# Kernel tuning notes

Measured on AMD Instinct MI355X. Metric: run time of the kernel, lower is better.

Reference implementation:

```python
import jax, jax.numpy as jnp
import numpy as np

N_POINTS = 32768
K = 16
N_EDGES = N_POINTS * K
IN_CH, OUT_CH = 3, 1
HID, LIFT, PROJ = 64, 256, 256
N_LAYERS = 4
POS_DIM = 2


def _lin_init(key, fan_in, fan_out):
    return jax.random.normal(key, (fan_in, fan_out), jnp.float32) / np.sqrt(fan_in)


def setup_inputs() -> dict:
    key = jax.random.key(0)
    ks = jax.random.split(key, 16)
    x = jax.random.normal(ks[0], (2, N_POINTS, IN_CH), jnp.float32)
    pos = jax.random.uniform(ks[1], (N_POINTS, POS_DIM), jnp.float32)
    edge_index = jax.random.randint(ks[2], (2, N_EDGES), 0, N_POINTS, jnp.int64)
    eff_in = IN_CH + POS_DIM
    kin = HID + 2 * POS_DIM  # concat(pos_src, pos_dst, x_src)
    return {
        "x": x,
        "pos": pos,
        "edge_index": edge_index,
        "lift_w1": _lin_init(ks[3], eff_in, LIFT),
        "lift_b1": jnp.zeros((LIFT,), jnp.float32),
        "lift_w2": _lin_init(ks[4], LIFT, HID),
        "lift_b2": jnp.zeros((HID,), jnp.float32),
        "kW1": jax.random.normal(ks[5], (N_LAYERS, kin, HID), jnp.float32) / np.sqrt(kin),
        "kb1": jnp.zeros((N_LAYERS, HID), jnp.float32),
        "kW2": jax.random.normal(ks[6], (N_LAYERS, HID, HID), jnp.float32) / np.sqrt(HID),
        "kb2": jnp.zeros((N_LAYERS, HID), jnp.float32),
        "proj_w1": _lin_init(ks[7], HID, PROJ),
        "proj_b1": jnp.zeros((PROJ,), jnp.float32),
        "proj_w2": _lin_init(ks[8], PROJ, OUT_CH),
        "proj_b2": jnp.zeros((OUT_CH,), jnp.float32),
    }


def _gelu(v):
    return jax.nn.gelu(v, approximate=False)  # torch nn.GELU default (exact)


def reference(x, pos, edge_index, lift_w1, lift_b1, lift_w2, lift_b2,
              kW1, kb1, kW2, kb2, proj_w1, proj_b1, proj_w2, proj_b2):
    B, n, _ = x.shape
    posb = jnp.broadcast_to(pos[None], (B, n, pos.shape[-1]))
    # lift: Linear -> GELU -> Linear on concat([x, pos])
    h = jnp.concatenate([x, posb], axis=-1)
    h = _gelu(h @ lift_w1 + lift_b1) @ lift_w2 + lift_b2  # [B, n, HID]

    src, dst = edge_index[0], edge_index[1]
    pos_e = jnp.concatenate([pos[src], pos[dst]], axis=-1)  # [E, 2*POS_DIM]
    cnt = jax.ops.segment_sum(jnp.ones((src.shape[0],), h.dtype), dst, num_segments=n)
    cnt = jnp.maximum(cnt, 1.0)[None, :, None]

    for l in range(kW1.shape[0]):
        xj = h[:, src]  # gather neighbor features [B, E, HID]
        e = jnp.concatenate([jnp.broadcast_to(pos_e[None], (B,) + pos_e.shape), xj], axis=-1)
        m = _gelu(e @ kW1[l] + kb1[l]) @ kW2[l] + kb2[l]  # edge messages [B, E, HID]
        agg = jax.vmap(lambda mb: jax.ops.segment_sum(mb, dst, num_segments=n))(m)
        h = h + agg / cnt  # mean aggregation + residual skip

    out = _gelu(h @ proj_w1 + proj_b1) @ proj_w2 + proj_b2  # [B, n, OUT_CH]
    return out.transpose(0, 2, 1)  # [B, OUT_CH, n]
```

## Files before the change

kernel.cpp:

```cpp
#include <hip/hip_runtime.h>
#include <cstdint>
#include <cstddef>

#define N_POINTS 32768
#define KDEG 16
#define N_EDGES (N_POINTS*KDEG)
#define BATCH 2
#define HID 64
#define LIFTD 256
#define PROJD 256
#define KIN 68
#define NLAYERS 4

#define DSTS 32
#define LK_WAVES 4
#define GSTR 72
#define MSTR 65

#define LASTR 40
#define LGSTR 264

#define FR_EDGE 0
#define FR_LW1  80
#define FR_LW2  96
#define FR_TOT  128

typedef unsigned short ushort_t;
typedef short short8 __attribute__((ext_vector_type(8)));
typedef float floatx4 __attribute__((ext_vector_type(4)));

union frag_u { uint4 u; short8 s; };

__device__ __forceinline__ float gelu_fast(float x) {
    float t = x * x;
    float inner = x * fmaf(0.044715f, t, 1.0f);
    float e = __expf(-1.5957691216f * inner);
#if __has_builtin(__builtin_amdgcn_rcpf)
    return x * __builtin_amdgcn_rcpf(1.0f + e);
#else
    return x * __frcp_rn(1.0f + e);
#endif
}

__device__ __forceinline__ ushort_t f2bf(float x) {
    return (ushort_t)((__float_as_uint(x) + 0x8000u) >> 16);
}
__device__ __forceinline__ unsigned int pk2bf(float a, float b) {
    return (unsigned int)f2bf(a) | ((unsigned int)f2bf(b) << 16);
}

__global__ void hist_kernel(const int* __restrict__ ei, int* __restrict__ counts) {
    int e = blockIdx.x * 256 + threadIdx.x;
    if (e < N_EDGES) atomicAdd(&counts[ei[N_EDGES + e]], 1);
}

__global__ void scan_kernel(const int* __restrict__ counts, int* __restrict__ row_start) {
    __shared__ int sums[1024];
    const int tid = threadIdx.x;
    const int base = tid * 32;
    int s = 0;
    for (int i = 0; i < 32; ++i) s += counts[base + i];
    sums[tid] = s;
    __syncthreads();
    const int own = s;
    for (int off = 1; off < 1024; off <<= 1) {
        int v = (tid >= off) ? sums[tid - off] : 0;
        __syncthreads();
        sums[tid] += v;
        __syncthreads();
    }
    int run = sums[tid] - own;
    for (int i = 0; i < 32; ++i) { row_start[base + i] = run; run += counts[base + i]; }
    if (tid == 1023) row_start[N_POINTS] = N_EDGES;
}

__global__ void fill_kernel(const int* __restrict__ ei, const int* __restrict__ row_start,
                            int* __restrict__ cursor, int2* __restrict__ csr_pair) {
    int e = blockIdx.x * 256 + threadIdx.x;
    if (e < N_EDGES) {
        int s = ei[e], d = ei[N_EDGES + e];
        int p = atomicAdd(&cursor[d], 1);
        csr_pair[row_start[d] + p] = make_int2(s, d);
    }
}

__global__ void wprep_kernel(const float* __restrict__ kW1, const float* __restrict__ kb1,
                             const float* __restrict__ kW2,
                             const float* __restrict__ lw1, const float* __restrict__ lb1,
                             const float* __restrict__ lw2,
                             ushort_t* __restrict__ wfrag) {
    int t = blockIdx.x * 256 + threadIdx.x;
    if (t >= FR_TOT * 64) return;
    const int lane = t & 63;
    const int fi = t >> 6;
    const int m16 = lane & 15;
    const int qb = ((lane >> 4) & 3) * 8;
    ushort_t o[8];
    if (fi < FR_LW1) {
        const int l = fi / 20, f = fi % 20;
        const int n = ((f < 12 ? (f & 3) : ((f - 12) & 3)) * 16) + m16;
        if (f < 12) {
            const int kc = f >> 2;
            const float* W1 = kW1 + (size_t)l * KIN * HID;
            const float* B1 = kb1 + (size_t)l * HID;
#pragma unroll
            for (int j = 0; j < 8; ++j) {
                const int k = kc * 32 + qb + j;
                float v;
                if (k < 64) v = W1[(size_t)(4 + k) * HID + n];
                else if (k < 68) v = W1[(size_t)(k - 64) * HID + n];
                else if (k == 68) v = B1[n];
                else v = 0.f;
                o[j] = f2bf(v);
            }
        } else {
            const int kc = (f - 12) >> 2;
            const float* W2 = kW2 + (size_t)l * HID * HID;
#pragma unroll
            for (int j = 0; j < 8; ++j)
                o[j] = f2bf(W2[(size_t)(kc * 32 + qb + j) * HID + n]);
        }
    } else if (fi < FR_LW2) {
        const int ct = fi - FR_LW1;
        const int n = ct * 16 + m16;
#pragma unroll
        for (int j = 0; j < 8; ++j) {
            const int k = qb + j;
            float v;
            if (k < 5) v = lw1[(size_t)k * LIFTD + n];
            else if (k == 5) v = lb1[n];
            else v = 0.f;
            o[j] = f2bf(v);
        }
    } else {
        const int idx = fi - FR_LW2;
        const int kc = idx >> 2, ct = idx & 3;
        const int n = ct * 16 + m16;
#pragma unroll
        for (int j = 0; j < 8; ++j)
            o[j] = f2bf(lw2[(size_t)(kc * 32 + qb + j) * HID + n]);
    }
    ushort_t* dst = wfrag + ((size_t)fi * 64 + lane) * 8;
#pragma unroll
    for (int j = 0; j < 8; ++j) dst[j] = o[j];
}

__global__ void wprep_proj_kernel(const float* __restrict__ pw1, ushort_t* __restrict__ pfrag) {
    int t = blockIdx.x * 256 + threadIdx.x;
    if (t >= 32 * 64) return;
    const int lane = t & 63;
    const int fi = t >> 6;
    const int kc = fi >> 4, ct = fi & 15;
    const int n = ct * 16 + (lane & 15);
    const int qb = ((lane >> 4) & 3) * 8;
    ushort_t* dst = pfrag + ((size_t)fi * 64 + lane) * 8;
#pragma unroll
    for (int j = 0; j < 8; ++j)
        dst[j] = f2bf(pw1[(size_t)(kc * 32 + qb + j) * PROJD + n]);
}

__global__ __launch_bounds__(256) void lift_kernel(
    const float* __restrict__ x, const float* __restrict__ pos,
    const ushort_t* __restrict__ wfrag, const float* __restrict__ lb2,
    float* __restrict__ hres, ushort_t* __restrict__ hb16)
{
    __shared__ __align__(16) ushort_t WF[3072 * 8];
    __shared__ __align__(16) ushort_t LA[4][16 * LASTR];
    __shared__ __align__(16) ushort_t LG[4][16 * LGSTR];

    const int tid = threadIdx.x;
    const int wv = tid >> 6;
    const int lane = tid & 63;
    const int m16 = lane & 15;
    const int q = lane >> 4;

    {
        const uint4* gw = (const uint4*)(wfrag + (size_t)FR_LW1 * 64 * 8);
        uint4* lw = (uint4*)WF;
        for (int i = tid; i < 3072; i += 256) lw[i] = gw[i];
    }
    __syncthreads();

    ushort_t* At = &LA[wv][0];
    ushort_t* Gt = &LG[wv][0];

    float b2r[4];
#pragma unroll
    for (int ct = 0; ct < 4; ++ct) b2r[ct] = lb2[ct * 16 + m16];

    for (int grp = 0; grp < 2; ++grp) {
        const int gid0 = (blockIdx.x * 8 + wv * 2 + grp) * 16;

        if (lane < 16) {
            const int g = gid0 + lane;
            const int i = g & (N_POINTS - 1);
            const float x0 = x[3 * (size_t)g], x1 = x[3 * (size_t)g + 1], x2 = x[3 * (size_t)g + 2];
            const float2 p = *(const float2*)(pos + 2 * i);
            uint4 w;
            w.x = pk2bf(x0, x1);
            w.y = pk2bf(x2, p.x);
            w.z = pk2bf(p.y, 1.0f);
            w.w = 0u;
            uint4 z; z.x = z.y = z.z = z.w = 0u;
            *(uint4*)&At[lane * LASTR + 0] = w;
            *(uint4*)&At[lane * LASTR + 8] = z;
            *(uint4*)&At[lane * LASTR + 16] = z;
            *(uint4*)&At[lane * LASTR + 24] = z;
        }

        const short8 a = *(const short8*)&At[m16 * LASTR + q * 8];
        floatx4 acc[16];
#pragma unroll
        for (int ct = 0; ct < 16; ++ct) {
            const short8 bf = *(const short8*)&WF[((size_t)ct * 64 + lane) * 8];
            floatx4 c = {0.f, 0.f, 0.f, 0.f};
            acc[ct] = __builtin_amdgcn_mfma_f32_16x16x32_bf16(a, bf, c, 0, 0, 0);
        }

#pragma unroll
        for (int ct = 0; ct < 16; ++ct)
#pragma unroll
            for (int r = 0; r < 4; ++r)
                Gt[(q * 4 + r) * LGSTR + ct * 16 + m16] = f2bf(gelu_fast(acc[ct][r]));

        floatx4 acc2[4];
#pragma unroll
        for (int ct = 0; ct < 4; ++ct) { floatx4 z = {0.f, 0.f, 0.f, 0.f}; acc2[ct] = z; }
#pragma unroll
        for (int kc = 0; kc < 8; ++kc) {
            const short8 g = *(const short8*)&Gt[m16 * LGSTR + kc * 32 + q * 8];
#pragma unroll
            for (int ct = 0; ct < 4; ++ct) {
                const short8 bf = *(const short8*)&WF[((size_t)(1024 + (kc * 4 + ct) * 64) + lane) * 8];
                acc2[ct] = __builtin_amdgcn_mfma_f32_16x16x32_bf16(g, bf, acc2[ct], 0, 0, 0);
            }
        }

#pragma unroll
        for (int ct = 0; ct < 4; ++ct)
#pragma unroll
            for (int r = 0; r < 4; ++r) {
                const float v = acc2[ct][r] + b2r[ct];
                const size_t idx = (size_t)(gid0 + q * 4 + r) * HID + ct * 16 + m16;
                hres[idx] = v;
                hb16[idx] = f2bf(v);
            }
    }
}

__global__ __launch_bounds__(256, 4) void layer_kernel(
    float* __restrict__ hres,
    const ushort_t* __restrict__ hb_in,
    ushort_t* __restrict__ hb_out,
    const float* __restrict__ pos,
    const int2* __restrict__ csr_pair,
    const int* __restrict__ row_start, const int* __restrict__ counts,
    const ushort_t* __restrict__ wfrag, const float* __restrict__ B2)
{
    __shared__ __align__(16) float GMt[LK_WAVES][16 * MSTR];
    __shared__ float hacc[DSTS * HID];
    __shared__ int   segb[LK_WAVES][16];

    const int b = blockIdx.y;
    const int dstBase = blockIdx.x * DSTS;
    const int tid = threadIdx.x;
    const int wv = tid >> 6;
    const int lane = tid & 63;
    const int m16 = lane & 15;
    const int q = lane >> 4;
    const int ch = lane & 3;
    const int growL = lane >> 2;
    const int permSrc = m16 * 4 + q;

    for (int i = tid; i < DSTS * HID; i += 256) hacc[i] = 0.f;

    const short8* wf = (const short8*)wfrag;
    short8 w1f[3][4], w2f[2][4];
#pragma unroll
    for (int kc = 0; kc < 3; ++kc)
#pragma unroll
        for (int ct = 0; ct < 4; ++ct) w1f[kc][ct] = wf[(kc * 4 + ct) * 64 + lane];
#pragma unroll
    for (int kc = 0; kc < 2; ++kc)
#pragma unroll
        for (int ct = 0; ct < 4; ++ct) w2f[kc][ct] = wf[(12 + kc * 4 + ct) * 64 + lane];
    __syncthreads();

    const int estart = row_start[dstBase];
    const int eend   = row_start[dstBase + DSTS];
    const int ntiles = (eend - estart + 15) >> 4;
    const int elast  = (eend > 0) ? (eend - 1) : 0;
    const ushort_t* __restrict__ hb = hb_in + (size_t)b * N_POINTS * HID;

    float* GM = &GMt[wv][0];
    ushort_t* Gt = (ushort_t*)GM;

    frag_u hC0, hC1; uint4 pwC; int segC;
    {
        const int e0 = estart + wv * 16;
        const int2 pA = csr_pair[min(e0 + growL, elast)];
        const int2 pB = csr_pair[min(e0 + m16, elast)];
        const uint4* hr = (const uint4*)(hb + (size_t)pA.x * HID);
        hC0.u = hr[ch];
        hC1.u = hr[ch + 4];
        const float2 ps = *(const float2*)(pos + 2 * pB.x);
        const float2 pd = *(const float2*)(pos + 2 * pB.y);
        pwC.x = pk2bf(ps.x, ps.y);
        pwC.y = pk2bf(pd.x, pd.y);
        pwC.z = 0x00003F80u;
        pwC.w = 0u;
        segC = (e0 + m16 < eend) ? (pB.y - dstBase) : -1;
    }

    for (int t = wv; t < ntiles; t += LK_WAVES) {
        frag_u hN0, hN1; uint4 pwN; int segN;
        {
            const int e0n = estart + (t + LK_WAVES) * 16;
            const int2 pA = csr_pair[min(e0n + growL, elast)];
            const int2 pB = csr_pair[min(e0n + m16, elast)];
            const uint4* hr = (const uint4*)(hb + (size_t)pA.x * HID);
            hN0.u = hr[ch];
            hN1.u = hr[ch + 4];
            const float2 ps = *(const float2*)(pos + 2 * pB.x);
            const float2 pd = *(const float2*)(pos + 2 * pB.y);
            pwN.x = pk2bf(ps.x, ps.y);
            pwN.y = pk2bf(pd.x, pd.y);
            pwN.z = 0x00003F80u;
            pwN.w = 0u;
            segN = (e0n + m16 < eend) ? (pB.y - dstBase) : -1;
        }

        if (lane < 16) segb[wv][lane] = segC;

        frag_u a0, a1, a2;
        a0.u.x = (unsigned)__shfl((int)hC0.u.x, permSrc);
        a0.u.y = (unsigned)__shfl((int)hC0.u.y, permSrc);
        a0.u.z = (unsigned)__shfl((int)hC0.u.z, permSrc);
        a0.u.w = (unsigned)__shfl((int)hC0.u.w, permSrc);
        a1.u.x = (unsigned)__shfl((int)hC1.u.x, permSrc);
        a1.u.y = (unsigned)__shfl((int)hC1.u.y, permSrc);
        a1.u.z = (unsigned)__shfl((int)hC1.u.z, permSrc);
        a1.u.w = (unsigned)__shfl((int)hC1.u.w, permSrc);
        if (q == 0) { a2.u = pwC; }
        else        { a2.u.x = 0u; a2.u.y = 0u; a2.u.z = 0u; a2.u.w = 0u; }

        floatx4 acc[4];
#pragma unroll
        for (int ct = 0; ct < 4; ++ct) {
            floatx4 c = {0.f, 0.f, 0.f, 0.f};
            c = __builtin_amdgcn_mfma_f32_16x16x32_bf16(a0.s, w1f[0][ct], c, 0, 0, 0);
            c = __builtin_amdgcn_mfma_f32_16x16x32_bf16(a1.s, w1f[1][ct], c, 0, 0, 0);
            c = __builtin_amdgcn_mfma_f32_16x16x32_bf16(a2.s, w1f[2][ct], c, 0, 0, 0);
            acc[ct] = c;
        }

#pragma unroll
        for (int ct = 0; ct < 4; ++ct)
#pragma unroll
            for (int r = 0; r < 4; ++r)
                Gt[(q * 4 + r) * GSTR + ct * 16 + m16] = f2bf(gelu_fast(acc[ct][r]));

        short8 g0 = *(const short8*)&Gt[m16 * GSTR +  0 + q * 8];
        short8 g1 = *(const short8*)&Gt[m16 * GSTR + 32 + q * 8];
        floatx4 mm[4];
#pragma unroll
        for (int ct = 0; ct < 4; ++ct) {
            floatx4 c = {0.f, 0.f, 0.f, 0.f};
            c = __builtin_amdgcn_mfma_f32_16x16x32_bf16(g0, w2f[0][ct], c, 0, 0, 0);
            c = __builtin_amdgcn_mfma_f32_16x16x32_bf16(g1, w2f[1][ct], c, 0, 0, 0);
            mm[ct] = c;
        }

#pragma unroll
        for (int ct = 0; ct < 4; ++ct)
#pragma unroll
            for (int r = 0; r < 4; ++r)
                GM[(q * 4 + r) * MSTR + ct * 16 + m16] = mm[ct][r];

        {
            float racc = 0.f;
            int rseg = -1;
#pragma unroll
            for (int r = 0; r < 16; ++r) {
                const int s = segb[wv][r];
                const float v = GM[r * MSTR + lane];
                if (s != rseg) {
                    if (rseg >= 0) atomicAdd(&hacc[rseg * HID + lane], racc);
                    rseg = s;
                    racc = v;
                } else {
                    racc += v;
                }
            }
            if (rseg >= 0) atomicAdd(&hacc[rseg * HID + lane], racc);
        }

        hC0 = hN0; hC1 = hN1; pwC = pwN; segC = segN;
    }
    __syncthreads();

    const size_t rowbase = (size_t)b * N_POINTS * HID;
    for (int i = tid; i < DSTS * HID; i += 256) {
        const int dl = i >> 6, c = i & 63;
        const int node = dstBase + dl;
        const int cntv = counts[node];
        const float cl = fmaxf((float)cntv, 1.f);
        const size_t off = rowbase + (size_t)node * HID + c;
        const float v = hres[off] + hacc[i] / cl + (cntv > 0 ? B2[c] : 0.f);
        hres[off] = v;
        hb_out[off] = f2bf(v);
    }
}

__global__ __launch_bounds__(256) void proj_kernel(
    const ushort_t* __restrict__ hbm, const ushort_t* __restrict__ pfrag,
    const float* __restrict__ b1, const float* __restrict__ w2,
    const float* __restrict__ b2, float* __restrict__ out)
{
    __shared__ __align__(16) ushort_t WF[2048 * 8];

    const int tid = threadIdx.x;
    const int wv = tid >> 6;
    const int lane = tid & 63;
    const int m16 = lane & 15;
    const int q = lane >> 4;

    {
        const uint4* gw = (const uint4*)pfrag;
        uint4* lw = (uint4*)WF;
        for (int i = tid; i < 2048; i += 256) lw[i] = gw[i];
    }
    __syncthreads();

    float b1v[16], w2v[16];
#pragma unroll
    for (int ct = 0; ct < 16; ++ct) {
        b1v[ct] = b1[ct * 16 + m16];
        w2v[ct] = w2[ct * 16 + m16];
    }
    const float b2s = b2[0];

    for (int grp = 0; grp < 2; ++grp) {
        const int gid0 = (blockIdx.x * 8 + wv * 2 + grp) * 16;

        frag_u a0, a1;
        const uint4* hr = (const uint4*)(hbm + (size_t)(gid0 + m16) * HID);
        a0.u = hr[q];
        a1.u = hr[4 + q];

        floatx4 acc[16];
#pragma unroll
        for (int ct = 0; ct < 16; ++ct) {
            const short8 bf0 = *(const short8*)&WF[((size_t)(ct) * 64 + lane) * 8];
            const short8 bf1 = *(const short8*)&WF[((size_t)(16 + ct) * 64 + lane) * 8];
            floatx4 c = {0.f, 0.f, 0.f, 0.f};
            c = __builtin_amdgcn_mfma_f32_16x16x32_bf16(a0.s, bf0, c, 0, 0, 0);
            c = __builtin_amdgcn_mfma_f32_16x16x32_bf16(a1.s, bf1, c, 0, 0, 0);
            acc[ct] = c;
        }

        float p[4] = {0.f, 0.f, 0.f, 0.f};
#pragma unroll
        for (int ct = 0; ct < 16; ++ct)
#pragma unroll
            for (int r = 0; r < 4; ++r)
                p[r] += gelu_fast(acc[ct][r] + b1v[ct]) * w2v[ct];

#pragma unroll
        for (int r = 0; r < 4; ++r) {
            p[r] += __shfl_xor(p[r], 1);
            p[r] += __shfl_xor(p[r], 2);
            p[r] += __shfl_xor(p[r], 4);
            p[r] += __shfl_xor(p[r], 8);
        }
        if (m16 == 0) {
#pragma unroll
            for (int r = 0; r < 4; ++r)
                out[gid0 + q * 4 + r] = p[r] + b2s;
        }
    }
}

extern "C" void kernel_launch(void* const* d_in, const int* in_sizes, int n_in,
                              void* d_out, int out_size, void* d_ws, size_t ws_size,
                              hipStream_t stream)
{
    const float* x        = (const float*)d_in[0];
    const float* pos      = (const float*)d_in[1];
    const int*   ei       = (const int*)d_in[2];
    const float* lift_w1  = (const float*)d_in[3];
    const float* lift_b1  = (const float*)d_in[4];
    const float* lift_w2  = (const float*)d_in[5];
    const float* lift_b2  = (const float*)d_in[6];
    const float* kW1      = (const float*)d_in[7];
    const float* kb1      = (const float*)d_in[8];
    const float* kW2      = (const float*)d_in[9];
    const float* kb2      = (const float*)d_in[10];
    const float* proj_w1  = (const float*)d_in[11];
    const float* proj_b1  = (const float*)d_in[12];
    const float* proj_w2  = (const float*)d_in[13];
    const float* proj_b2  = (const float*)d_in[14];
    float* out = (float*)d_out;

    char* ws = (char*)d_ws;
    size_t off = 0;
    float*    hres  = (float*)(ws + off);    off += (size_t)BATCH * N_POINTS * HID * 4;
    ushort_t* hbA   = (ushort_t*)(ws + off); off += (size_t)BATCH * N_POINTS * HID * 2;
    ushort_t* hbB   = (ushort_t*)(ws + off); off += (size_t)BATCH * N_POINTS * HID * 2;
    int* counts     = (int*)(ws + off);      off += (size_t)N_POINTS * 4;
    int* row_start  = (int*)(ws + off);      off += (size_t)(N_POINTS + 4) * 4;
    int* cursor     = (int*)(ws + off);      off += (size_t)N_POINTS * 4;
    int2* csr_pair  = (int2*)(ws + off);     off += (size_t)N_EDGES * 8;
    ushort_t* wfrag = (ushort_t*)cursor;
    ushort_t* pfrag = (ushort_t*)csr_pair;

    hipMemsetAsync(counts, 0, N_POINTS * 4, stream);
    hipMemsetAsync(cursor, 0, N_POINTS * 4, stream);

    hist_kernel<<<N_EDGES / 256, 256, 0, stream>>>(ei, counts);
    scan_kernel<<<1, 1024, 0, stream>>>(counts, row_start);
    fill_kernel<<<N_EDGES / 256, 256, 0, stream>>>(ei, row_start, cursor, csr_pair);
    wprep_kernel<<<(FR_TOT * 64) / 256, 256, 0, stream>>>(
        kW1, kb1, kW2, lift_w1, lift_b1, lift_w2, wfrag);

    lift_kernel<<<BATCH * N_POINTS / 128, 256, 0, stream>>>(x, pos, wfrag, lift_b2, hres, hbA);

    ushort_t* hin = hbA;
    ushort_t* hout = hbB;
    for (int l = 0; l < NLAYERS; ++l) {
        layer_kernel<<<dim3(N_POINTS / DSTS, BATCH), 256, 0, stream>>>(
            hres, hin, hout, pos, csr_pair, row_start, counts,
            wfrag + (size_t)l * 20 * 64 * 8, kb2 + (size_t)l * HID);
        ushort_t* tmp = hin; hin = hout; hout = tmp;
    }

    wprep_proj_kernel<<<(32 * 64) / 256, 256, 0, stream>>>(proj_w1, pfrag);
    proj_kernel<<<BATCH * N_POINTS / 128, 256, 0, stream>>>(
        hin, pfrag, proj_b1, proj_w2, proj_b2, out);
}
```

Baseline: 592.1 us.

## Process both batch elements per layer block to share CSR, pos and weight loads

The layer kernel now handles both batch elements in one block instead of using a grid dimension per batch. Each edge tile's CSR pair, position data, weight fragments and segment ids are loaded once and reused for both batches, and the shared accumulator doubles in size. The grid halves, which removes redundant index and weight traffic but raises register pressure from the doubled prefetch buffers and LDS use, possibly lowering occupancy.

```diff
diff --git a/kernel.cpp b/kernel.cpp
--- a/kernel.cpp
+++ b/kernel.cpp
@@ -258,10 +258,9 @@
     const ushort_t* __restrict__ wfrag, const float* __restrict__ B2)
 {
     __shared__ __align__(16) float GMt[LK_WAVES][16 * MSTR];
-    __shared__ float hacc[DSTS * HID];
+    __shared__ float hacc[BATCH * DSTS * HID];
     __shared__ int   segb[LK_WAVES][16];
 
-    const int b = blockIdx.y;
     const int dstBase = blockIdx.x * DSTS;
     const int tid = threadIdx.x;
     const int wv = tid >> 6;
@@ -272,7 +271,7 @@
     const int growL = lane >> 2;
     const int permSrc = m16 * 4 + q;
 
-    for (int i = tid; i < DSTS * HID; i += 256) hacc[i] = 0.f;
+    for (int i = tid; i < BATCH * DSTS * HID; i += 256) hacc[i] = 0.f;
 
     const short8* wf = (const short8*)wfrag;
     short8 w1f[3][4], w2f[2][4];
@@ -290,19 +289,22 @@
     const int eend   = row_start[dstBase + DSTS];
     const int ntiles = (eend - estart + 15) >> 4;
     const int elast  = (eend > 0) ? (eend - 1) : 0;
-    const ushort_t* __restrict__ hb = hb_in + (size_t)b * N_POINTS * HID;
+    const ushort_t* __restrict__ hb0 = hb_in;
+    const ushort_t* __restrict__ hb1 = hb_in + (size_t)N_POINTS * HID;
 
     float* GM = &GMt[wv][0];
     ushort_t* Gt = (ushort_t*)GM;
 
-    frag_u hC0, hC1; uint4 pwC; int segC;
+    frag_u hC0[2], hC1[2]; uint4 pwC; int segC;
     {
         const int e0 = estart + wv * 16;
         const int2 pA = csr_pair[min(e0 + growL, elast)];
         const int2 pB = csr_pair[min(e0 + m16, elast)];
-        const uint4* hr = (const uint4*)(hb + (size_t)pA.x * HID);
-        hC0.u = hr[ch];
-        hC1.u = hr[ch + 4];
+        const size_t rowoff = (size_t)pA.x * HID;
+        const uint4* hr0 = (const uint4*)(hb0 + rowoff);
+        const uint4* hr1 = (const uint4*)(hb1 + rowoff);
+        hC0[0].u = hr0[ch]; hC1[0].u = hr0[ch + 4];
+        hC0[1].u = hr1[ch]; hC1[1].u = hr1[ch + 4];
         const float2 ps = *(const float2*)(pos + 2 * pB.x);
         const float2 pd = *(const float2*)(pos + 2 * pB.y);
         pwC.x = pk2bf(ps.x, ps.y);
@@ -313,14 +315,16 @@
     }
 
     for (int t = wv; t < ntiles; t += LK_WAVES) {
-        frag_u hN0, hN1; uint4 pwN; int segN;
+        frag_u hN0[2], hN1[2]; uint4 pwN; int segN;
         {
             const int e0n = estart + (t + LK_WAVES) * 16;
             const int2 pA = csr_pair[min(e0n + growL, elast)];
             const int2 pB = csr_pair[min(e0n + m16, elast)];
-            const uint4* hr = (const uint4*)(hb + (size_t)pA.x * HID);
-            hN0.u = hr[ch];
-            hN1.u = hr[ch + 4];
+            const size_t rowoff = (size_t)pA.x * HID;
+            const uint4* hr0 = (const uint4*)(hb0 + rowoff);
+            const uint4* hr1 = (const uint4*)(hb1 + rowoff);
+            hN0[0].u = hr0[ch]; hN1[0].u = hr0[ch + 4];
+            hN0[1].u = hr1[ch]; hN1[1].u = hr1[ch + 4];
             const float2 ps = *(const float2*)(pos + 2 * pB.x);
             const float2 pd = *(const float2*)(pos + 2 * pB.y);
             pwN.x = pk2bf(ps.x, ps.y);
@@ -332,80 +336,89 @@
 
         if (lane < 16) segb[wv][lane] = segC;
 
-        frag_u a0, a1, a2;
-        a0.u.x = (unsigned)__shfl((int)hC0.u.x, permSrc);
-        a0.u.y = (unsigned)__shfl((int)hC0.u.y, permSrc);
-        a0.u.z = (unsigned)__shfl((int)hC0.u.z, permSrc);
-        a0.u.w = (unsigned)__shfl((int)hC0.u.w, permSrc);
-        a1.u.x = (unsigned)__shfl((int)hC1.u.x, permSrc);
-        a1.u.y = (unsigned)__shfl((int)hC1.u.y, permSrc);
-        a1.u.z = (unsigned)__shfl((int)hC1.u.z, permSrc);
-        a1.u.w = (unsigned)__shfl((int)hC1.u.w, permSrc);
+        frag_u a2;
         if (q == 0) { a2.u = pwC; }
         else        { a2.u.x = 0u; a2.u.y = 0u; a2.u.z = 0u; a2.u.w = 0u; }
 
-        floatx4 acc[4];
-#pragma unroll
-        for (int ct = 0; ct < 4; ++ct) {
-            floatx4 c = {0.f, 0.f, 0.f, 0.f};
-            c = __builtin_amdgcn_mfma_f32_16x16x32_bf16(a0.s, w1f[0][ct], c, 0, 0, 0);
-            c = __builtin_amdgcn_mfma_f32_16x16x32_bf16(a1.s, w1f[1][ct], c, 0, 0, 0);
-            c = __builtin_amdgcn_mfma_f32_16x16x32_bf16(a2.s, w1f[2][ct], c, 0, 0, 0);
-            acc[ct] = c;
-        }
-
-#pragma unroll
-        for (int ct = 0; ct < 4; ++ct)
-#pragma unroll
-            for (int r = 0; r < 4; ++r)
-                Gt[(q * 4 + r) * GSTR + ct * 16 + m16] = f2bf(gelu_fast(acc[ct][r]));
-
-        short8 g0 = *(const short8*)&Gt[m16 * GSTR +  0 + q * 8];
-        short8 g1 = *(const short8*)&Gt[m16 * GSTR + 32 + q * 8];
-        floatx4 mm[4];
-#pragma unroll
-        for (int ct = 0; ct < 4; ++ct) {
-            floatx4 c = {0.f, 0.f, 0.f, 0.f};
-            c = __builtin_amdgcn_mfma_f32_16x16x32_bf16(g0, w2f[0][ct], c, 0, 0, 0);
-            c = __builtin_amdgcn_mfma_f32_16x16x32_bf16(g1, w2f[1][ct], c, 0, 0, 0);
-            mm[ct] = c;
-        }
-
-#pragma unroll
-        for (int ct = 0; ct < 4; ++ct)
-#pragma unroll
-            for (int r = 0; r < 4; ++r)
-                GM[(q * 4 + r) * MSTR + ct * 16 + m16] = mm[ct][r];
-
-        {
-            float racc = 0.f;
-            int rseg = -1;
-#pragma unroll
-            for (int r = 0; r < 16; ++r) {
-                const int s = segb[wv][r];
-                const float v = GM[r * MSTR + lane];
-                if (s != rseg) {
-                    if (rseg >= 0) atomicAdd(&hacc[rseg * HID + lane], racc);
-                    rseg = s;
-                    racc = v;
-                } else {
-                    racc += v;
+#pragma unroll
+        for (int bb = 0; bb < BATCH; ++bb) {
+            frag_u a0, a1;
+            a0.u.x = (unsigned)__shfl((int)hC0[bb].u.x, permSrc);
+            a0.u.y = (unsigned)__shfl((int)hC0[bb].u.y, permSrc);
+            a0.u.z = (unsigned)__shfl((int)hC0[bb].u.z, permSrc);
+            a0.u.w = (unsigned)__shfl((int)hC0[bb].u.w, permSrc);
+            a1.u.x = (unsigned)__shfl((int)hC1[bb].u.x, permSrc);
+            a1.u.y = (unsigned)__shfl((int)hC1[bb].u.y, permSrc);
+            a1.u.z = (unsigned)__shfl((int)hC1[bb].u.z, permSrc);
+            a1.u.w = (unsigned)__shfl((int)hC1[bb].u.w, permSrc);
+
+            floatx4 acc[4];
+#pragma unroll
+            for (int ct = 0; ct < 4; ++ct) {
+                floatx4 c = {0.f, 0.f, 0.f, 0.f};
+                c = __builtin_amdgcn_mfma_f32_16x16x32_bf16(a0.s, w1f[0][ct], c, 0, 0, 0);
+                c = __builtin_amdgcn_mfma_f32_16x16x32_bf16(a1.s, w1f[1][ct], c, 0, 0, 0);
+                c = __builtin_amdgcn_mfma_f32_16x16x32_bf16(a2.s, w1f[2][ct], c, 0, 0, 0);
+                acc[ct] = c;
+            }
+
+#pragma unroll
+            for (int ct = 0; ct < 4; ++ct)
+#pragma unroll
+                for (int r = 0; r < 4; ++r)
+                    Gt[(q * 4 + r) * GSTR + ct * 16 + m16] = f2bf(gelu_fast(acc[ct][r]));
+
+            short8 g0 = *(const short8*)&Gt[m16 * GSTR +  0 + q * 8];
+            short8 g1 = *(const short8*)&Gt[m16 * GSTR + 32 + q * 8];
+            floatx4 mm[4];
+#pragma unroll
+            for (int ct = 0; ct < 4; ++ct) {
+                floatx4 c = {0.f, 0.f, 0.f, 0.f};
+                c = __builtin_amdgcn_mfma_f32_16x16x32_bf16(g0, w2f[0][ct], c, 0, 0, 0);
+                c = __builtin_amdgcn_mfma_f32_16x16x32_bf16(g1, w2f[1][ct], c, 0, 0, 0);
+                mm[ct] = c;
+            }
+
+#pragma unroll
+            for (int ct = 0; ct < 4; ++ct)
+#pragma unroll
+                for (int r = 0; r < 4; ++r)
+                    GM[(q * 4 + r) * MSTR + ct * 16 + m16] = mm[ct][r];
+
+            {
+                float* hca = &hacc[bb * DSTS * HID];
+                float racc = 0.f;
+                int rseg = -1;
+#pragma unroll
+                for (int r = 0; r < 16; ++r) {
+                    const int s = segb[wv][r];
+                    const float v = GM[r * MSTR + lane];
+                    if (s != rseg) {
+                        if (rseg >= 0) atomicAdd(&hca[rseg * HID + lane], racc);
+                        rseg = s;
+                        racc = v;
+                    } else {
+                        racc += v;
+                    }
                 }
+                if (rseg >= 0) atomicAdd(&hca[rseg * HID + lane], racc);
             }
-            if (rseg >= 0) atomicAdd(&hacc[rseg * HID + lane], racc);
-        }
-
-        hC0 = hN0; hC1 = hN1; pwC = pwN; segC = segN;
+        }
+
+        hC0[0] = hN0[0]; hC1[0] = hN1[0];
+        hC0[1] = hN0[1]; hC1[1] = hN1[1];
+        pwC = pwN; segC = segN;
     }
     __syncthreads();
 
-    const size_t rowbase = (size_t)b * N_POINTS * HID;
-    for (int i = tid; i < DSTS * HID; i += 256) {
-        const int dl = i >> 6, c = i & 63;
+    for (int i = tid; i < BATCH * DSTS * HID; i += 256) {
+        const int bb = i >> 11;
+        const int j = i & 2047;
+        const int dl = j >> 6, c = j & 63;
         const int node = dstBase + dl;
         const int cntv = counts[node];
         const float cl = fmaxf((float)cntv, 1.f);
-        const size_t off = rowbase + (size_t)node * HID + c;
+        const size_t off = (size_t)bb * N_POINTS * HID + (size_t)node * HID + c;
         const float v = hres[off] + hacc[i] / cl + (cntv > 0 ? B2[c] : 0.f);
         hres[off] = v;
         hb_out[off] = f2bf(v);
@@ -528,7 +541,7 @@
     ushort_t* hin = hbA;
     ushort_t* hout = hbB;
     for (int l = 0; l < NLAYERS; ++l) {
-        layer_kernel<<<dim3(N_POINTS / DSTS, BATCH), 256, 0, stream>>>(
+        layer_kernel<<<N_POINTS / DSTS, 256, 0, stream>>>(
             hres, hin, hout, pos, csr_pair, row_start, counts,
             wfrag + (size_t)l * 20 * 64 * 8, kb2 + (size_t)l * HID);
         ushort_t* tmp = hin; hin = hout; hout = tmp;
```

Result: slower. 669.8 us (+13.1%).
